# Kernel optimization log

Hardware: AMD Instinct MI355X
Metric: run time of the kernel (lower is better)

The kernel has to match this reference:

```python
import jax, jax.numpy as jnp
import numpy as np


def setup_inputs() -> dict:
    key = jax.random.key(0)
    k1, k2 = jax.random.split(key)
    B, S, H, E = 4, 4096, 4096, 64
    hidden_states = jax.random.normal(k1, (B, S, H), dtype=jnp.float32)
    W = jax.random.normal(k2, (E, H), dtype=jnp.float32) * 0.02  # nn.init.normal_(std=0.02)
    b = jnp.zeros((E,), dtype=jnp.float32)
    return {"hidden_states": hidden_states, "W": W, "b": b, "k": 2}


def reference(hidden_states, W, b, k):
    # Linear gating: [B,S,H] @ [H,E] + [E] -> [B,S,E]
    router_logits = jnp.einsum("bsh,eh->bse", hidden_states, W) + b
    # jitter noise is 0.0 -> no-op
    n_experts = W.shape[0]
    kk = min(k, n_experts)
    expert_weights, expert_indices = jax.lax.top_k(router_logits, kk)  # [B,S,k]
    expert_weights = jax.nn.softmax(expert_weights, axis=-1)
    return (router_logits, expert_indices, expert_weights)
```

## Files before the change

### kernel.cpp

```cpp
#include <hip/hip_runtime.h>
#include <math.h>


namespace {

constexpr int Hdim = 4096;
constexpr int Edim = 64;
constexpr int BM   = 64;
constexpr int BK   = 32;
constexpr int LDT  = 68;
constexpr int TILE = BK * LDT;

__global__ __launch_bounds__(256)
void router_kernel(const float* __restrict__ hid,
                   const float* __restrict__ Wm,
                   const float* __restrict__ bias,
                   float* __restrict__ out,
                   int nrows)
{
    __shared__ float smem[4 * TILE];
    float* sA = smem;
    float* sB = smem + 2 * TILE;

    const int tid = threadIdx.x;
    const int tx  = tid & 15;
    const int ty  = tid >> 4;
    const int rowBase = blockIdx.x * BM;

    const int srow = tid >> 3;
    const int skq  = (tid & 7) * 4;

    const float* aptr0 = hid + (size_t)(rowBase + srow) * Hdim + skq;
    const float* aptr1 = aptr0 + (size_t)32 * Hdim;
    const float* bptr0 = Wm  + (size_t)srow * Hdim + skq;
    const float* bptr1 = bptr0 + (size_t)32 * Hdim;

    float4 ra0, ra1, rb0, rb1;

    ra0 = *(const float4*)(aptr0);
    ra1 = *(const float4*)(aptr1);
    rb0 = *(const float4*)(bptr0);
    rb1 = *(const float4*)(bptr1);

    auto store_tile = [&](int buf) {
        float* A = sA + buf * TILE;
        float* B = sB + buf * TILE;
        A[(skq + 0) * LDT + srow]      = ra0.x;
        A[(skq + 1) * LDT + srow]      = ra0.y;
        A[(skq + 2) * LDT + srow]      = ra0.z;
        A[(skq + 3) * LDT + srow]      = ra0.w;
        A[(skq + 0) * LDT + srow + 32] = ra1.x;
        A[(skq + 1) * LDT + srow + 32] = ra1.y;
        A[(skq + 2) * LDT + srow + 32] = ra1.z;
        A[(skq + 3) * LDT + srow + 32] = ra1.w;
        B[(skq + 0) * LDT + srow]      = rb0.x;
        B[(skq + 1) * LDT + srow]      = rb0.y;
        B[(skq + 2) * LDT + srow]      = rb0.z;
        B[(skq + 3) * LDT + srow]      = rb0.w;
        B[(skq + 0) * LDT + srow + 32] = rb1.x;
        B[(skq + 1) * LDT + srow + 32] = rb1.y;
        B[(skq + 2) * LDT + srow + 32] = rb1.z;
        B[(skq + 3) * LDT + srow + 32] = rb1.w;
    };

    store_tile(0);
    __syncthreads();

    float acc[4][4];
    #pragma unroll
    for (int i = 0; i < 4; ++i)
        #pragma unroll
        for (int j = 0; j < 4; ++j) acc[i][j] = 0.0f;

    constexpr int NSTEP = Hdim / BK;
    for (int step = 0; step < NSTEP; ++step) {
        const int cur = step & 1;
        const bool more = (step + 1) < NSTEP;
        if (more) {
            const int off = (step + 1) * BK;
            ra0 = *(const float4*)(aptr0 + off);
            ra1 = *(const float4*)(aptr1 + off);
            rb0 = *(const float4*)(bptr0 + off);
            rb1 = *(const float4*)(bptr1 + off);
        }

        const float* A = sA + cur * TILE + ty * 4;
        const float* B = sB + cur * TILE + tx * 4;
        #pragma unroll 8
        for (int kk = 0; kk < BK; ++kk) {
            float4 a = *(const float4*)(A + kk * LDT);
            float4 b = *(const float4*)(B + kk * LDT);
            acc[0][0] = fmaf(a.x, b.x, acc[0][0]);
            acc[0][1] = fmaf(a.x, b.y, acc[0][1]);
            acc[0][2] = fmaf(a.x, b.z, acc[0][2]);
            acc[0][3] = fmaf(a.x, b.w, acc[0][3]);
            acc[1][0] = fmaf(a.y, b.x, acc[1][0]);
            acc[1][1] = fmaf(a.y, b.y, acc[1][1]);
            acc[1][2] = fmaf(a.y, b.z, acc[1][2]);
            acc[1][3] = fmaf(a.y, b.w, acc[1][3]);
            acc[2][0] = fmaf(a.z, b.x, acc[2][0]);
            acc[2][1] = fmaf(a.z, b.y, acc[2][1]);
            acc[2][2] = fmaf(a.z, b.z, acc[2][2]);
            acc[2][3] = fmaf(a.z, b.w, acc[2][3]);
            acc[3][0] = fmaf(a.w, b.x, acc[3][0]);
            acc[3][1] = fmaf(a.w, b.y, acc[3][1]);
            acc[3][2] = fmaf(a.w, b.z, acc[3][2]);
            acc[3][3] = fmaf(a.w, b.w, acc[3][3]);
        }

        if (more) store_tile(cur ^ 1);
        __syncthreads();
    }

    const float4 bvec = *(const float4*)(bias + tx * 4);
    float* lvals = smem;

    #pragma unroll
    for (int r = 0; r < 4; ++r) {
        float4 v;
        v.x = acc[r][0] + bvec.x;
        v.y = acc[r][1] + bvec.y;
        v.z = acc[r][2] + bvec.z;
        v.w = acc[r][3] + bvec.w;
        const int row = ty * 4 + r;
        *(float4*)(out + (size_t)(rowBase + row) * Edim + tx * 4) = v;
        *(float4*)(lvals + row * LDT + tx * 4) = v;
    }
    __syncthreads();

    if (tid < BM) {
        const float* lr = lvals + tid * LDT;
        float m1 = lr[0]; int i1 = 0;
        #pragma unroll 8
        for (int e = 1; e < Edim; ++e) {
            float v = lr[e];
            if (v > m1) { m1 = v; i1 = e; }
        }
        float m2 = -INFINITY; int i2 = 0;
        #pragma unroll 8
        for (int e = 0; e < Edim; ++e) {
            if (e == i1) continue;
            float v = lr[e];
            if (v > m2) { m2 = v; i2 = e; }
        }
        const float t  = expf(m2 - m1);
        const float w1 = 1.0f / (1.0f + t);
        const float w2 = t * w1;

        const size_t ro    = (size_t)(rowBase + tid);
        const size_t base2 = (size_t)nrows * Edim;
        const size_t base3 = base2 + (size_t)nrows * 2;
        out[base2 + ro * 2 + 0] = (float)i1;
        out[base2 + ro * 2 + 1] = (float)i2;
        out[base3 + ro * 2 + 0] = w1;
        out[base3 + ro * 2 + 1] = w2;
    }
}

}

extern "C" void kernel_launch(void* const* d_in, const int* in_sizes, int n_in,
                              void* d_out, int out_size, void* d_ws, size_t ws_size,
                              hipStream_t stream) {
    const float* hid  = (const float*)d_in[0];
    const float* Wm   = (const float*)d_in[1];
    const float* bias = (const float*)d_in[2];
    float* out = (float*)d_out;

    const int nrows = in_sizes[0] / Hdim;
    dim3 grid(nrows / BM);
    router_kernel<<<grid, 256, 0, stream>>>(hid, Wm, bias, out, nrows);
}
```

Measured before the change: 436.2 us.

## Replace FP32 SIMT GEMM with split-bf16x3 MFMA and split-K waves

Moves the router GEMM from scalar FMA tiles onto bf16 MFMA instructions. Each fp32 operand is split into three bf16 parts, and six cross products are accumulated to approximate fp32 precision. W is pre-split once per call into a workspace by a small conversion kernel. Each block handles 16 rows, with K split across 4 waves and reduced in shared memory; the output layout is recovered through an identity MFMA probe. This trades extra MFMA work and split arithmetic for far higher matrix throughput. It also reads hidden states straight from global memory without LDS staging.

```diff
diff --git a/kernel.cpp b/kernel.cpp
--- a/kernel.cpp
+++ b/kernel.cpp
@@ -4,144 +4,160 @@
 
 namespace {
 
-constexpr int Hdim = 4096;
-constexpr int Edim = 64;
-constexpr int BM   = 64;
-constexpr int BK   = 32;
-constexpr int LDT  = 68;
-constexpr int TILE = BK * LDT;
+constexpr int Hdim  = 4096;
+constexpr int Edim  = 64;
+constexpr int RPB   = 16;
+constexpr int KW    = Hdim / 4;
+constexpr int PLANE = Edim * Hdim;
+
+typedef __attribute__((ext_vector_type(4))) float f32x4;
+typedef __attribute__((ext_vector_type(8))) short bf16x8;
+
+__device__ __forceinline__ void split3(float x, unsigned& h, unsigned& m, unsigned& l) {
+    unsigned uh = __float_as_uint(x);
+    h = uh >> 16;
+    float r1 = x - __uint_as_float(uh & 0xFFFF0000u);
+    unsigned um = __float_as_uint(r1);
+    m = um >> 16;
+    float r2 = r1 - __uint_as_float(um & 0xFFFF0000u);
+    l = __float_as_uint(r2) >> 16;
+}
+
+__device__ __forceinline__ short ftob(float x) {
+    return (short)(__float_as_uint(x) >> 16);
+}
 
 __global__ __launch_bounds__(256)
-void router_kernel(const float* __restrict__ hid,
-                   const float* __restrict__ Wm,
-                   const float* __restrict__ bias,
-                   float* __restrict__ out,
-                   int nrows)
+void convert_w3(const float* __restrict__ W, unsigned short* __restrict__ wsp) {
+    const int i = blockIdx.x * 256 + threadIdx.x;
+    unsigned h, m, l;
+    split3(W[i], h, m, l);
+    wsp[i]             = (unsigned short)h;
+    wsp[PLANE + i]     = (unsigned short)m;
+    wsp[2 * PLANE + i] = (unsigned short)l;
+}
+
+template <bool PRE>
+__global__ __launch_bounds__(256)
+void router_mfma(const float* __restrict__ hid,
+                 const void* __restrict__ Wsrc,
+                 const float* __restrict__ bias,
+                 float* __restrict__ out, int nrows)
 {
-    __shared__ float smem[4 * TILE];
-    float* sA = smem;
-    float* sB = smem + 2 * TILE;
+    __shared__ float red[4][RPB][Edim + 4];
+    __shared__ float fin[RPB][Edim + 1];
 
-    const int tid = threadIdx.x;
-    const int tx  = tid & 15;
-    const int ty  = tid >> 4;
-    const int rowBase = blockIdx.x * BM;
+    const int tid  = threadIdx.x;
+    const int wave = tid >> 6;
+    const int lane = tid & 63;
+    const int l15  = lane & 15;
+    const int lk   = lane >> 4;
+    const int rowBase = blockIdx.x * RPB;
+    const int k0 = wave * KW + lk * 8;
 
-    const int srow = tid >> 3;
-    const int skq  = (tid & 7) * 4;
+    bf16x8 aid, benc;
+    #pragma unroll
+    for (int e = 0; e < 8; ++e) {
+        const int kl = lk * 8 + e;
+        aid[e]  = ftob(kl == l15 ? 1.0f : 0.0f);
+        benc[e] = ftob(kl < 16 ? (float)(kl * 16 + l15) : 0.0f);
+    }
+    f32x4 pr = (f32x4){0.f, 0.f, 0.f, 0.f};
+    pr = __builtin_amdgcn_mfma_f32_16x16x32_bf16(aid, benc, pr, 0, 0, 0);
+    int prow[4], pcol[4];
+    #pragma unroll
+    for (int r = 0; r < 4; ++r) {
+        const int code = (int)pr[r];
+        prow[r] = (code >> 4) & 15;
+        pcol[r] = code & 15;
+    }
 
-    const float* aptr0 = hid + (size_t)(rowBase + srow) * Hdim + skq;
-    const float* aptr1 = aptr0 + (size_t)32 * Hdim;
-    const float* bptr0 = Wm  + (size_t)srow * Hdim + skq;
-    const float* bptr1 = bptr0 + (size_t)32 * Hdim;
+    const float* aptr = hid + (size_t)(rowBase + l15) * Hdim + k0;
 
-    float4 ra0, ra1, rb0, rb1;
+    f32x4 acc[4];
+    #pragma unroll
+    for (int t = 0; t < 4; ++t) acc[t] = (f32x4){0.f, 0.f, 0.f, 0.f};
 
-    ra0 = *(const float4*)(aptr0);
-    ra1 = *(const float4*)(aptr1);
-    rb0 = *(const float4*)(bptr0);
-    rb1 = *(const float4*)(bptr1);
+    for (int s = 0; s < KW / 32; ++s) {
+        f32x4 a0 = *(const f32x4*)(aptr);
+        f32x4 a1 = *(const f32x4*)(aptr + 4);
+        aptr += 32;
+        bf16x8 ah, am, al;
+        #pragma unroll
+        for (int j = 0; j < 4; ++j) {
+            unsigned h, m, l;
+            split3(a0[j], h, m, l);
+            ah[j] = (short)h;  am[j] = (short)m;  al[j] = (short)l;
+            split3(a1[j], h, m, l);
+            ah[4 + j] = (short)h;  am[4 + j] = (short)m;  al[4 + j] = (short)l;
+        }
 
-    auto store_tile = [&](int buf) {
-        float* A = sA + buf * TILE;
-        float* B = sB + buf * TILE;
-        A[(skq + 0) * LDT + srow]      = ra0.x;
-        A[(skq + 1) * LDT + srow]      = ra0.y;
-        A[(skq + 2) * LDT + srow]      = ra0.z;
-        A[(skq + 3) * LDT + srow]      = ra0.w;
-        A[(skq + 0) * LDT + srow + 32] = ra1.x;
-        A[(skq + 1) * LDT + srow + 32] = ra1.y;
-        A[(skq + 2) * LDT + srow + 32] = ra1.z;
-        A[(skq + 3) * LDT + srow + 32] = ra1.w;
-        B[(skq + 0) * LDT + srow]      = rb0.x;
-        B[(skq + 1) * LDT + srow]      = rb0.y;
-        B[(skq + 2) * LDT + srow]      = rb0.z;
-        B[(skq + 3) * LDT + srow]      = rb0.w;
-        B[(skq + 0) * LDT + srow + 32] = rb1.x;
-        B[(skq + 1) * LDT + srow + 32] = rb1.y;
-        B[(skq + 2) * LDT + srow + 32] = rb1.z;
-        B[(skq + 3) * LDT + srow + 32] = rb1.w;
-    };
+        #pragma unroll
+        for (int t = 0; t < 4; ++t) {
+            bf16x8 bh, bm, bl;
+            if (PRE) {
+                const unsigned short* wsp = (const unsigned short*)Wsrc;
+                const size_t boff = (size_t)(l15 + 16 * t) * Hdim + k0 + s * 32;
+                bh = *(const bf16x8*)(wsp + boff);
+                bm = *(const bf16x8*)(wsp + PLANE + boff);
+                bl = *(const bf16x8*)(wsp + 2 * PLANE + boff);
+            } else {
+                const float* wf = (const float*)Wsrc
+                                + (size_t)(l15 + 16 * t) * Hdim + k0 + s * 32;
+                f32x4 b0 = *(const f32x4*)(wf);
+                f32x4 b1 = *(const f32x4*)(wf + 4);
+                #pragma unroll
+                for (int j = 0; j < 4; ++j) {
+                    unsigned h, m, l;
+                    split3(b0[j], h, m, l);
+                    bh[j] = (short)h;  bm[j] = (short)m;  bl[j] = (short)l;
+                    split3(b1[j], h, m, l);
+                    bh[4 + j] = (short)h;  bm[4 + j] = (short)m;  bl[4 + j] = (short)l;
+                }
+            }
+            acc[t] = __builtin_amdgcn_mfma_f32_16x16x32_bf16(al, bh, acc[t], 0, 0, 0);
+            acc[t] = __builtin_amdgcn_mfma_f32_16x16x32_bf16(am, bm, acc[t], 0, 0, 0);
+            acc[t] = __builtin_amdgcn_mfma_f32_16x16x32_bf16(ah, bl, acc[t], 0, 0, 0);
+            acc[t] = __builtin_amdgcn_mfma_f32_16x16x32_bf16(am, bh, acc[t], 0, 0, 0);
+            acc[t] = __builtin_amdgcn_mfma_f32_16x16x32_bf16(ah, bm, acc[t], 0, 0, 0);
+            acc[t] = __builtin_amdgcn_mfma_f32_16x16x32_bf16(ah, bh, acc[t], 0, 0, 0);
+        }
+    }
 
-    store_tile(0);
+    #pragma unroll
+    for (int t = 0; t < 4; ++t)
+        #pragma unroll
+        for (int r = 0; r < 4; ++r)
+            red[wave][prow[r]][t * 16 + pcol[r]] = acc[t][r];
+
     __syncthreads();
 
-    float acc[4][4];
     #pragma unroll
-    for (int i = 0; i < 4; ++i)
-        #pragma unroll
-        for (int j = 0; j < 4; ++j) acc[i][j] = 0.0f;
-
-    constexpr int NSTEP = Hdim / BK;
-    for (int step = 0; step < NSTEP; ++step) {
-        const int cur = step & 1;
-        const bool more = (step + 1) < NSTEP;
-        if (more) {
-            const int off = (step + 1) * BK;
-            ra0 = *(const float4*)(aptr0 + off);
-            ra1 = *(const float4*)(aptr1 + off);
-            rb0 = *(const float4*)(bptr0 + off);
-            rb1 = *(const float4*)(bptr1 + off);
-        }
-
-        const float* A = sA + cur * TILE + ty * 4;
-        const float* B = sB + cur * TILE + tx * 4;
-        #pragma unroll 8
-        for (int kk = 0; kk < BK; ++kk) {
-            float4 a = *(const float4*)(A + kk * LDT);
-            float4 b = *(const float4*)(B + kk * LDT);
-            acc[0][0] = fmaf(a.x, b.x, acc[0][0]);
-            acc[0][1] = fmaf(a.x, b.y, acc[0][1]);
-            acc[0][2] = fmaf(a.x, b.z, acc[0][2]);
-            acc[0][3] = fmaf(a.x, b.w, acc[0][3]);
-            acc[1][0] = fmaf(a.y, b.x, acc[1][0]);
-            acc[1][1] = fmaf(a.y, b.y, acc[1][1]);
-            acc[1][2] = fmaf(a.y, b.z, acc[1][2]);
-            acc[1][3] = fmaf(a.y, b.w, acc[1][3]);
-            acc[2][0] = fmaf(a.z, b.x, acc[2][0]);
-            acc[2][1] = fmaf(a.z, b.y, acc[2][1]);
-            acc[2][2] = fmaf(a.z, b.z, acc[2][2]);
-            acc[2][3] = fmaf(a.z, b.w, acc[2][3]);
-            acc[3][0] = fmaf(a.w, b.x, acc[3][0]);
-            acc[3][1] = fmaf(a.w, b.y, acc[3][1]);
-            acc[3][2] = fmaf(a.w, b.z, acc[3][2]);
-            acc[3][3] = fmaf(a.w, b.w, acc[3][3]);
-        }
-
-        if (more) store_tile(cur ^ 1);
-        __syncthreads();
-    }
-
-    const float4 bvec = *(const float4*)(bias + tx * 4);
-    float* lvals = smem;
-
-    #pragma unroll
-    for (int r = 0; r < 4; ++r) {
-        float4 v;
-        v.x = acc[r][0] + bvec.x;
-        v.y = acc[r][1] + bvec.y;
-        v.z = acc[r][2] + bvec.z;
-        v.w = acc[r][3] + bvec.w;
-        const int row = ty * 4 + r;
-        *(float4*)(out + (size_t)(rowBase + row) * Edim + tx * 4) = v;
-        *(float4*)(lvals + row * LDT + tx * 4) = v;
+    for (int j = 0; j < 4; ++j) {
+        const int e   = tid + j * 256;
+        const int row = e >> 6;
+        const int col = e & 63;
+        float v = red[0][row][col] + red[1][row][col]
+                + red[2][row][col] + red[3][row][col] + bias[col];
+        out[(size_t)(rowBase + row) * Edim + col] = v;
+        fin[row][col] = v;
     }
     __syncthreads();
 
-    if (tid < BM) {
-        const float* lr = lvals + tid * LDT;
+    if (tid < RPB) {
+        const float* lr = &fin[tid][0];
         float m1 = lr[0]; int i1 = 0;
         #pragma unroll 8
-        for (int e = 1; e < Edim; ++e) {
-            float v = lr[e];
-            if (v > m1) { m1 = v; i1 = e; }
+        for (int e2 = 1; e2 < Edim; ++e2) {
+            float v = lr[e2];
+            if (v > m1) { m1 = v; i1 = e2; }
         }
         float m2 = -INFINITY; int i2 = 0;
         #pragma unroll 8
-        for (int e = 0; e < Edim; ++e) {
-            if (e == i1) continue;
-            float v = lr[e];
-            if (v > m2) { m2 = v; i2 = e; }
+        for (int e2 = 0; e2 < Edim; ++e2) {
+            if (e2 == i1) continue;
+            float v = lr[e2];
+            if (v > m2) { m2 = v; i2 = e2; }
         }
         const float t  = expf(m2 - m1);
         const float w1 = 1.0f / (1.0f + t);
@@ -167,7 +183,13 @@
     const float* bias = (const float*)d_in[2];
     float* out = (float*)d_out;
 
-    const int nrows = in_sizes[0] / Hdim;
-    dim3 grid(nrows / BM);
-    router_kernel<<<grid, 256, 0, stream>>>(hid, Wm, bias, out, nrows);
+    const int nrows   = in_sizes[0] / Hdim;
+    const int nblocks = nrows / RPB;
+
+    if (ws_size >= (size_t)(3 * PLANE * sizeof(unsigned short))) {
+        convert_w3<<<PLANE / 256, 256, 0, stream>>>(Wm, (unsigned short*)d_ws);
+        router_mfma<true><<<nblocks, 256, 0, stream>>>(hid, d_ws, bias, out, nrows);
+    } else {
+        router_mfma<false><<<nblocks, 256, 0, stream>>>(hid, Wm, bias, out, nrows);
+    }
 }
```

After: 521.2 us. +19.5%, slower.
